# Kernel tuning notes

Hardware: AMD Instinct MI355X
Metric: run time of the kernel (lower is better)

The kernel has to match this reference:

```python
import jax, jax.numpy as jnp
import numpy as np

B, N, D = 8, 2048, 256
SCALE = 10.0  # self.scale_constant

def setup_inputs() -> dict:
    key = jax.random.key(0)
    ks = jax.random.split(key, 8)
    x = jax.random.normal(ks[0], (B, N, D), dtype=jnp.float32)
    recycler_mask = jax.random.randint(ks[1], (N, N), 0, 2, dtype=jnp.int32)
    s = 1.0 / np.sqrt(D)
    Wq = jax.random.uniform(ks[2], (D, D), jnp.float32, -s, s)
    bq = jax.random.uniform(ks[3], (D,), jnp.float32, -s, s)
    Wk = jax.random.uniform(ks[4], (D, D), jnp.float32, -s, s)
    bk = jax.random.uniform(ks[5], (D,), jnp.float32, -s, s)
    Wl = jax.random.uniform(ks[6], (1, D), jnp.float32, -s, s)
    bl = jax.random.uniform(ks[7], (1,), jnp.float32, -s, s)
    return {"x": x, "recycler_mask": recycler_mask, "Wq": Wq, "bq": bq,
            "Wk": Wk, "bk": bk, "Wl": Wl, "bl": bl}

def reference(x, recycler_mask, Wq, bq, Wk, bk, Wl, bl):
    # query/key linear projections (torch Linear: x @ W.T + b)
    query = jnp.einsum('bnd,ed->bne', x, Wq) + bq  # (B,N,D)
    key_ = jnp.einsum('bnd,ed->bne', x, Wk) + bk   # (B,N,D)
    scores = jnp.einsum('bnd,bmd->bnm', query, key_)  # (B,N,N)
    scores = SCALE * jnp.tanh(scores)
    scores = jnp.where(recycler_mask[None, :, :] == 0, -jnp.inf, scores)
    picked_logit = jnp.einsum('bnd,ed->bne', x, Wl) + bl  # (B,N,1)
    return picked_logit, scores
```

## Files before the change

kernel.cpp:

```cpp
#include <hip/hip_runtime.h>
#include <math.h>

#define B_ 8
#define N_ 2048
#define D_ 256
#define SCALE_ 10.0f
#define NEG_SENTINEL_ (-1.0e30f)

#define BM 128
#define BN 128
#define BK 64
#define KTILES (D_ / BK)
#define TILE_ELEMS (BM * BK)

typedef unsigned short ushort_t;
typedef unsigned long long u64_t;
typedef __attribute__((ext_vector_type(8))) short bf16x8;
typedef __attribute__((ext_vector_type(4))) float f32x4;

__device__ __forceinline__ ushort_t f2bf(float f) {
    union { float f; unsigned int u; } a; a.f = f;
    unsigned int r = a.u + 0x7fffu + ((a.u >> 16) & 1u);
    return (ushort_t)(r >> 16);
}

__device__ __forceinline__ void gl16(const void* g, void* l) {
    __builtin_amdgcn_global_load_lds(
        (const __attribute__((address_space(1))) unsigned int*)g,
        (__attribute__((address_space(3))) unsigned int*)l, 16, 0, 0);
}


__global__ __launch_bounds__(256) void rcy_proj_v6(
    const float* __restrict__ x,
    const float* __restrict__ Wq, const float* __restrict__ bq,
    const float* __restrict__ Wk, const float* __restrict__ bk,
    const float* __restrict__ Wl, const float* __restrict__ bl,
    ushort_t* __restrict__ Qo, ushort_t* __restrict__ Ko,
    float* __restrict__ logit)
{
    __shared__ ushort_t As[BM * BK];
    __shared__ ushort_t Bqs[BN * BK];
    __shared__ ushort_t Bks[BN * BK];

    const int m0 = blockIdx.x * BM;
    const int n0 = blockIdx.y * BN;
    const int t  = threadIdx.x;
    const int w  = t >> 6, l = t & 63;
    const int wr = w >> 1, wc = w & 1;
    const int srow0 = t >> 3;
    const int schunk = t & 7;
    const bool do_logit = (blockIdx.y == 0);

    f32x4 accq[4][4] = {};
    f32x4 acck[4][4] = {};
    float lacc[4] = {0.f, 0.f, 0.f, 0.f};

    for (int k0 = 0; k0 < D_; k0 += BK) {
        __syncthreads();
        float4 wl0, wl1;
        if (do_logit) {
            const float4* wlp = (const float4*)(Wl + k0 + schunk * 8);
            wl0 = wlp[0]; wl1 = wlp[1];
        }
        #pragma unroll
        for (int p = 0; p < 4; ++p) {
            const int row = p * 32 + srow0;
            const int off = ((row * 128 + schunk * 16) ^ ((row & 7) << 4));
            const float4* xa = (const float4*)(x + (size_t)(m0 + row) * D_ + k0 + schunk * 8);
            float4 f0 = xa[0], f1 = xa[1];
            union { bf16x8 v; ushort_t u[8]; } pa;
            pa.u[0]=f2bf(f0.x); pa.u[1]=f2bf(f0.y); pa.u[2]=f2bf(f0.z); pa.u[3]=f2bf(f0.w);
            pa.u[4]=f2bf(f1.x); pa.u[5]=f2bf(f1.y); pa.u[6]=f2bf(f1.z); pa.u[7]=f2bf(f1.w);
            *(bf16x8*)((char*)As + off) = pa.v;
            if (do_logit) {
                lacc[p] += f0.x*wl0.x + f0.y*wl0.y + f0.z*wl0.z + f0.w*wl0.w
                         + f1.x*wl1.x + f1.y*wl1.y + f1.z*wl1.z + f1.w*wl1.w;
            }
            const float4* qa = (const float4*)(Wq + (size_t)(n0 + row) * D_ + k0 + schunk * 8);
            float4 g0 = qa[0], g1 = qa[1];
            union { bf16x8 v; ushort_t u[8]; } pb;
            pb.u[0]=f2bf(g0.x); pb.u[1]=f2bf(g0.y); pb.u[2]=f2bf(g0.z); pb.u[3]=f2bf(g0.w);
            pb.u[4]=f2bf(g1.x); pb.u[5]=f2bf(g1.y); pb.u[6]=f2bf(g1.z); pb.u[7]=f2bf(g1.w);
            *(bf16x8*)((char*)Bqs + off) = pb.v;
            const float4* ka = (const float4*)(Wk + (size_t)(n0 + row) * D_ + k0 + schunk * 8);
            float4 h0 = ka[0], h1 = ka[1];
            union { bf16x8 v; ushort_t u[8]; } pc;
            pc.u[0]=f2bf(h0.x); pc.u[1]=f2bf(h0.y); pc.u[2]=f2bf(h0.z); pc.u[3]=f2bf(h0.w);
            pc.u[4]=f2bf(h1.x); pc.u[5]=f2bf(h1.y); pc.u[6]=f2bf(h1.z); pc.u[7]=f2bf(h1.w);
            *(bf16x8*)((char*)Bks + off) = pc.v;
        }
        __syncthreads();
        #pragma unroll
        for (int ks = 0; ks < 2; ++ks) {
            bf16x8 af[4], bqf[4], bkf[4];
            #pragma unroll
            for (int f = 0; f < 4; ++f) {
                const int m = wr * 64 + f * 16 + (l & 15);
                const int aoff = ((m * 128 + ks * 64 + (l >> 4) * 16) ^ ((m & 7) << 4));
                af[f] = *(const bf16x8*)((const char*)As + aoff);
                const int n = wc * 64 + f * 16 + (l & 15);
                const int boff = ((n * 128 + ks * 64 + (l >> 4) * 16) ^ ((n & 7) << 4));
                bqf[f] = *(const bf16x8*)((const char*)Bqs + boff);
                bkf[f] = *(const bf16x8*)((const char*)Bks + boff);
            }
            #pragma unroll
            for (int i = 0; i < 4; ++i)
                #pragma unroll
                for (int j = 0; j < 4; ++j) {
                    accq[i][j] = __builtin_amdgcn_mfma_f32_16x16x32_bf16(af[i], bqf[j], accq[i][j], 0, 0, 0);
                    acck[i][j] = __builtin_amdgcn_mfma_f32_16x16x32_bf16(af[i], bkf[j], acck[i][j], 0, 0, 0);
                }
        }
    }

    const int b  = m0 >> 11;
    const int rb = (m0 & 2047) >> 7;
    const size_t tbase = (((size_t)b * 16 + rb) * KTILES + (blockIdx.y * 2 + wc)) * (size_t)TILE_ELEMS;
    #pragma unroll
    for (int j = 0; j < 4; ++j) {
        const int col = n0 + wc * 64 + j * 16 + (l & 15);
        const float bvq = bq[col];
        const float bvk = bk[col];
        const int cl = j * 16 + (l & 15);
        #pragma unroll
        for (int i = 0; i < 4; ++i) {
            #pragma unroll
            for (int r = 0; r < 4; ++r) {
                const int rl = wr * 64 + i * 16 + (l >> 4) * 4 + r;
                const int sidx = (rl * BK + cl) ^ ((rl & 7) << 3);
                Qo[tbase + (size_t)sidx] = f2bf(accq[i][j][r] + bvq);
                Ko[tbase + (size_t)sidx] = f2bf(acck[i][j][r] + bvk);
            }
        }
    }

    if (do_logit) {
        const float bl0 = bl[0];
        #pragma unroll
        for (int p = 0; p < 4; ++p) {
            float s = lacc[p];
            s += __shfl_down(s, 4);
            s += __shfl_down(s, 2);
            s += __shfl_down(s, 1);
            if (schunk == 0) logit[m0 + p * 32 + srow0] = s + bl0;
        }
    }
}

__global__ __launch_bounds__(256) void rcy_maskpack(
    const int* __restrict__ mask, u64_t* __restrict__ bits)
{
    const int gid = blockIdx.x * 256 + threadIdx.x;
    const u64_t bal = __ballot(mask[gid] != 0);
    if ((threadIdx.x & 63) == 0) bits[gid >> 6] = bal;
}

__global__ __launch_bounds__(256) void rcy_scores_v9(
    const ushort_t* __restrict__ Qt, const ushort_t* __restrict__ Kt,
    const u64_t* __restrict__ bits, float* __restrict__ out)
{
    __shared__ ushort_t lds[2][2][TILE_ELEMS];
    __shared__ u64_t bitlds[256];

    const int g  = blockIdx.x;
    const int bz = g >> 8;
    const int r_ = g & 255;
    const int grp = r_ >> 4;
    const int within = r_ & 15;
    const int bx = (grp & 3) * 4 + (within & 3);
    const int by = (grp >> 2) * 4 + (within >> 2);
    const int t  = threadIdx.x;
    const int w  = t >> 6, l = t & 63;
    const int wr = w >> 1, wc = w & 1;

    const char* gA = (const char*)(Qt + (((size_t)bz * 16 + bx) * KTILES) * TILE_ELEMS);
    const char* gB = (const char*)(Kt + (((size_t)bz * 16 + by) * KTILES) * TILE_ELEMS);

    const u64_t mybits = bits[(size_t)(bx * BM + (t >> 1)) * (N_ / 64) + by * 2 + (t & 1)];

    f32x4 acc[4][4] = {};

    #define STAGE(buf, kb) { \
        const char* sa = gA + (size_t)(kb) * (TILE_ELEMS * 2); \
        const char* sb = gB + (size_t)(kb) * (TILE_ELEMS * 2); \
        char* la = (char*)&lds[buf][0][0]; \
        char* lb = (char*)&lds[buf][1][0]; \
        _Pragma("unroll") \
        for (int q = 0; q < 4; ++q) { \
            gl16(sa + q * 4096 + t * 16, la + q * 4096 + t * 16); \
            gl16(sb + q * 4096 + t * 16, lb + q * 4096 + t * 16); \
        } }

    #define COMPUTE(buf) { \
        const char* As_ = (const char*)&lds[buf][0][0]; \
        const char* Bs_ = (const char*)&lds[buf][1][0]; \
        _Pragma("unroll") \
        for (int ks = 0; ks < 2; ++ks) { \
            bf16x8 af[4], bf[4]; \
            _Pragma("unroll") \
            for (int f = 0; f < 4; ++f) { \
                const int m = wr * 64 + f * 16 + (l & 15); \
                const int aoff = (m * 128 + ks * 64 + (l >> 4) * 16) ^ ((m & 7) << 4); \
                af[f] = *(const bf16x8*)(As_ + aoff); \
                const int n = wc * 64 + f * 16 + (l & 15); \
                const int boff = (n * 128 + ks * 64 + (l >> 4) * 16) ^ ((n & 7) << 4); \
                bf[f] = *(const bf16x8*)(Bs_ + boff); \
            } \
            _Pragma("unroll") \
            for (int i = 0; i < 4; ++i) \
                _Pragma("unroll") \
                for (int j = 0; j < 4; ++j) \
                    acc[i][j] = __builtin_amdgcn_mfma_f32_16x16x32_bf16(af[i], bf[j], acc[i][j], 0, 0, 0); \
        } }

    STAGE(0, 0);
    STAGE(1, 1);
    asm volatile("s_waitcnt vmcnt(8)" ::: "memory");
    __builtin_amdgcn_s_barrier();
    COMPUTE(0);
    __builtin_amdgcn_s_barrier();
    STAGE(0, 2);
    asm volatile("s_waitcnt vmcnt(8)" ::: "memory");
    __builtin_amdgcn_s_barrier();
    COMPUTE(1);
    __builtin_amdgcn_s_barrier();
    STAGE(1, 3);
    asm volatile("s_waitcnt vmcnt(8)" ::: "memory");
    __builtin_amdgcn_s_barrier();
    COMPUTE(0);
    __builtin_amdgcn_s_barrier();
    asm volatile("s_waitcnt vmcnt(0)" ::: "memory");
    __builtin_amdgcn_s_barrier();
    COMPUTE(1);
    bitlds[t] = mybits;
    __syncthreads();

    const int bm0 = bx * BM, bn0 = by * BN;
    float* outb = out + (size_t)bz * N_ * N_;
    #pragma unroll
    for (int i = 0; i < 4; ++i) {
        #pragma unroll
        for (int r = 0; r < 4; ++r) {
            const int rl = wr * 64 + i * 16 + (l >> 4) * 4 + r;
            const u64_t mrow = bitlds[rl * 2 + wc];
            const int row = bm0 + rl;
            #pragma unroll
            for (int j = 0; j < 4; ++j) {
                const int col = bn0 + wc * 64 + j * 16 + (l & 15);
                const int mk = (int)((mrow >> (j * 16 + (l & 15))) & 1ull);
                const float v = acc[i][j][r];
                const float e = __expf(v + v);
                const float s = fmaf(-20.0f, __builtin_amdgcn_rcpf(e + 1.0f), SCALE_);
                outb[(size_t)row * N_ + col] = mk ? s : NEG_SENTINEL_;
            }
        }
    }
    #undef STAGE
    #undef COMPUTE
}

extern "C" void kernel_launch(void* const* d_in, const int* in_sizes, int n_in,
                              void* d_out, int out_size, void* d_ws, size_t ws_size,
                              hipStream_t stream)
{
    const float* x  = (const float*)d_in[0];
    const int* mask = (const int*)d_in[1];
    const float* Wq = (const float*)d_in[2];
    const float* bq = (const float*)d_in[3];
    const float* Wk = (const float*)d_in[4];
    const float* bk = (const float*)d_in[5];
    const float* Wl = (const float*)d_in[6];
    const float* bl = (const float*)d_in[7];

    float* logit  = (float*)d_out;
    float* scores = (float*)d_out + (size_t)B_ * N_;

    ushort_t* Qw = (ushort_t*)d_ws;
    ushort_t* Kw = Qw + (size_t)B_ * 16 * KTILES * TILE_ELEMS;
    u64_t* bits  = (u64_t*)(Kw + (size_t)B_ * 16 * KTILES * TILE_ELEMS);

    rcy_maskpack<<<dim3((N_*N_)/256), 256, 0, stream>>>(mask, bits);
    rcy_proj_v6<<<dim3((B_*N_)/BM, D_/BN), 256, 0, stream>>>(
        x, Wq, bq, Wk, bk, Wl, bl, Qw, Kw, logit);
    rcy_scores_v9<<<dim3((N_/BM) * (N_/BN) * B_), 256, 0, stream>>>(Qw, Kw, bits, scores);
}
```

Measured before the change: 68.25 us.

## Enlarge scores tile to 256x256 with 512-thread blocks and 3D grid

The scores kernel now computes a 256x256 output tile per block using 8 waves, each owning 128x64, and stages two 128-row sub-tiles of Q and K per k-step. The goal is more MFMA work per LDS load and less redundant global traffic for Q/K. The mask bits now live in the reused operand LDS buffer instead of a separate array. The L2-friendly swizzled block ordering is replaced by a plain 3D grid. The 128KB LDS footprint limits residency to one block per CU, and only 512 blocks remain, which risks tail imbalance in a kernel that is mostly bound by output stores.

Result: slower. 77.95 us (+14.2%).

```diff
diff --git a/kernel.cpp b/kernel.cpp
--- a/kernel.cpp
+++ b/kernel.cpp
@@ -156,59 +156,60 @@
     if ((threadIdx.x & 63) == 0) bits[gid >> 6] = bal;
 }
 
-__global__ __launch_bounds__(256) void rcy_scores_v9(
+__global__ __launch_bounds__(512) void rcy_scores_v10(
     const ushort_t* __restrict__ Qt, const ushort_t* __restrict__ Kt,
     const u64_t* __restrict__ bits, float* __restrict__ out)
 {
-    __shared__ ushort_t lds[2][2][TILE_ELEMS];
-    __shared__ u64_t bitlds[256];
-
-    const int g  = blockIdx.x;
-    const int bz = g >> 8;
-    const int r_ = g & 255;
-    const int grp = r_ >> 4;
-    const int within = r_ & 15;
-    const int bx = (grp & 3) * 4 + (within & 3);
-    const int by = (grp >> 2) * 4 + (within >> 2);
+    __shared__ ushort_t lds[2][2][2 * TILE_ELEMS];
+
+    const int bx = blockIdx.x;
+    const int by = blockIdx.y;
+    const int bz = blockIdx.z;
     const int t  = threadIdx.x;
     const int w  = t >> 6, l = t & 63;
-    const int wr = w >> 1, wc = w & 1;
-
-    const char* gA = (const char*)(Qt + (((size_t)bz * 16 + bx) * KTILES) * TILE_ELEMS);
-    const char* gB = (const char*)(Kt + (((size_t)bz * 16 + by) * KTILES) * TILE_ELEMS);
-
-    const u64_t mybits = bits[(size_t)(bx * BM + (t >> 1)) * (N_ / 64) + by * 2 + (t & 1)];
-
-    f32x4 acc[4][4] = {};
+    const int wr = w >> 2, wc = w & 3;
+
+    const size_t bidx = (size_t)(bx * 256 + (t >> 1)) * (N_ / 64) + by * 4 + (t & 1) * 2;
+    const u64_t mb0 = bits[bidx];
+    const u64_t mb1 = bits[bidx + 1];
+
+    f32x4 acc[8][4] = {};
 
     #define STAGE(buf, kb) { \
-        const char* sa = gA + (size_t)(kb) * (TILE_ELEMS * 2); \
-        const char* sb = gB + (size_t)(kb) * (TILE_ELEMS * 2); \
-        char* la = (char*)&lds[buf][0][0]; \
-        char* lb = (char*)&lds[buf][1][0]; \
         _Pragma("unroll") \
-        for (int q = 0; q < 4; ++q) { \
-            gl16(sa + q * 4096 + t * 16, la + q * 4096 + t * 16); \
-            gl16(sb + q * 4096 + t * 16, lb + q * 4096 + t * 16); \
-        } }
+        for (int h = 0; h < 2; ++h) { \
+            const char* sa = (const char*)(Qt + (((size_t)bz * 16 + 2 * bx + h) * KTILES + (kb)) * TILE_ELEMS); \
+            const char* sb = (const char*)(Kt + (((size_t)bz * 16 + 2 * by + h) * KTILES + (kb)) * TILE_ELEMS); \
+            char* la = (char*)&lds[buf][0][0] + h * 16384; \
+            char* lb = (char*)&lds[buf][1][0] + h * 16384; \
+            _Pragma("unroll") \
+            for (int q = 0; q < 2; ++q) { \
+                gl16(sa + q * 8192 + t * 16, la + q * 8192 + t * 16); \
+                gl16(sb + q * 8192 + t * 16, lb + q * 8192 + t * 16); \
+            } } }
 
     #define COMPUTE(buf) { \
         const char* As_ = (const char*)&lds[buf][0][0]; \
         const char* Bs_ = (const char*)&lds[buf][1][0]; \
         _Pragma("unroll") \
         for (int ks = 0; ks < 2; ++ks) { \
-            bf16x8 af[4], bf[4]; \
+            bf16x8 af[8], bf[4]; \
+            _Pragma("unroll") \
+            for (int f = 0; f < 8; ++f) { \
+                const int m = wr * 128 + f * 16 + (l & 15); \
+                const int mr = m & 127; \
+                const int aoff = (m >> 7) * 16384 + ((mr * 128 + ks * 64 + (l >> 4) * 16) ^ ((mr & 7) << 4)); \
+                af[f] = *(const bf16x8*)(As_ + aoff); \
+            } \
             _Pragma("unroll") \
             for (int f = 0; f < 4; ++f) { \
-                const int m = wr * 64 + f * 16 + (l & 15); \
-                const int aoff = (m * 128 + ks * 64 + (l >> 4) * 16) ^ ((m & 7) << 4); \
-                af[f] = *(const bf16x8*)(As_ + aoff); \
                 const int n = wc * 64 + f * 16 + (l & 15); \
-                const int boff = (n * 128 + ks * 64 + (l >> 4) * 16) ^ ((n & 7) << 4); \
+                const int nr = n & 127; \
+                const int boff = (n >> 7) * 16384 + ((nr * 128 + ks * 64 + (l >> 4) * 16) ^ ((nr & 7) << 4)); \
                 bf[f] = *(const bf16x8*)(Bs_ + boff); \
             } \
             _Pragma("unroll") \
-            for (int i = 0; i < 4; ++i) \
+            for (int i = 0; i < 8; ++i) \
                 _Pragma("unroll") \
                 for (int j = 0; j < 4; ++j) \
                     acc[i][j] = __builtin_amdgcn_mfma_f32_16x16x32_bf16(af[i], bf[j], acc[i][j], 0, 0, 0); \
@@ -232,18 +233,23 @@
     __builtin_amdgcn_s_barrier();
     asm volatile("s_waitcnt vmcnt(0)" ::: "memory");
     __builtin_amdgcn_s_barrier();
+    {
+        u64_t* bb = (u64_t*)&lds[0][0][0];
+        const int bi = (t >> 1) * 4 + (t & 1) * 2;
+        bb[bi] = mb0; bb[bi + 1] = mb1;
+    }
     COMPUTE(1);
-    bitlds[t] = mybits;
     __syncthreads();
 
-    const int bm0 = bx * BM, bn0 = by * BN;
+    const u64_t* bb = (const u64_t*)&lds[0][0][0];
+    const int bm0 = bx * 256, bn0 = by * 256;
     float* outb = out + (size_t)bz * N_ * N_;
     #pragma unroll
-    for (int i = 0; i < 4; ++i) {
+    for (int i = 0; i < 8; ++i) {
         #pragma unroll
         for (int r = 0; r < 4; ++r) {
-            const int rl = wr * 64 + i * 16 + (l >> 4) * 4 + r;
-            const u64_t mrow = bitlds[rl * 2 + wc];
+            const int rl = wr * 128 + i * 16 + (l >> 4) * 4 + r;
+            const u64_t mrow = bb[rl * 4 + wc];
             const int row = bm0 + rl;
             #pragma unroll
             for (int j = 0; j < 4; ++j) {
@@ -283,5 +289,5 @@
     rcy_maskpack<<<dim3((N_*N_)/256), 256, 0, stream>>>(mask, bits);
     rcy_proj_v6<<<dim3((B_*N_)/BM, D_/BN), 256, 0, stream>>>(
         x, Wq, bq, Wk, bk, Wl, bl, Qw, Kw, logit);
-    rcy_scores_v9<<<dim3((N_/BM) * (N_/BN) * B_), 256, 0, stream>>>(Qw, Kw, bits, scores);
-}
+    rcy_scores_v10<<<dim3(N_/256, N_/256, B_), 512, 0, stream>>>(Qw, Kw, bits, scores);
+}
```
